# Optimization experiments

Measured on AMD Instinct MI355X. Metric: run time of the kernel, lower is better.

## Reference

```python
import jax, jax.numpy as jnp
import numpy as np

MAX_SHIFT = 64  # init kwarg; alpha=None -> score_max branch


def setup_inputs() -> dict:
    key = jax.random.key(0)
    k1, k2 = jax.random.split(key)
    x = jax.random.normal(k1, (64, 2, 4096), dtype=jnp.float32)
    y = jax.random.normal(k2, (64, 2, 4096), dtype=jnp.float32)
    return {"x": x, "y": y}


def reference(x, y):
    S = MAX_SHIFT
    W = 2 * S + 1  # num_windows
    # forward(): flip along channel axis
    x = jnp.flip(x, axis=1)
    B, C, D = x.shape
    # min-max normalize each (batch, channel) trace to [-1, 1]
    xmin = x.min(axis=-1, keepdims=True)
    xmax = x.max(axis=-1, keepdims=True)
    x = 2 * (x - xmin) / (xmax - xmin) - 1
    # torch.hann_window(dim) is periodic: 0.5*(1 - cos(2*pi*n/N))
    hann = 0.5 * (1.0 - jnp.cos(2.0 * jnp.pi * jnp.arange(D, dtype=x.dtype) / D))
    x = x * hann
    # pad by max_shift on both sides, then take W sliding windows of length D
    xpad = jnp.pad(x, ((0, 0), (0, 0), (S, S)))  # [B, C, D+2S]
    idx = jnp.arange(W)[:, None] + jnp.arange(D)[None, :]  # [W, D]
    xw = xpad[:, :, idx]  # [B, C, W, D] (matches torch unfold+reshape)
    xw = jnp.transpose(xw, (2, 0, 1, 3))  # [W, B, C, D]
    # mean-centered Pearson correlation per window
    xc = xw - xw.mean(axis=-1, keepdims=True)
    yc = y - y.mean(axis=-1, keepdims=True)
    corr = jnp.sum(xc * yc, axis=-1)  # [W, B, C]
    norm = jnp.sum(xc * xc, axis=-1) * jnp.sum(yc * yc, axis=-1)
    corr = corr / jnp.sqrt(norm)
    # alpha is None -> score_max: max over shifts, L2 over channels
    values = corr.max(axis=0)  # [B, C]
    scores = jnp.sqrt(jnp.sum(values ** 2, axis=-1))  # [B]
    return -scores.mean()
```

## Files before the change

### kernel.cpp

```cpp
#include <hip/hip_runtime.h>
#include <math.h>

#define DD      4096
#define WW      129
#define XSN     4240
#define BLOCKN  256
#define NBLK    512

__device__ float g_part[NBLK];
__device__ int   g_cnt = 0;

__global__ __launch_bounds__(BLOCKN) void spl_fused(
        const float* __restrict__ x, const float* __restrict__ y,
        float* __restrict__ out) {
    const int blk = blockIdx.x;
    const int bc  = blk >> 2, p = blk & 3;
    const int b   = bc >> 1,  c = bc & 1;
    const float* xp = x + (size_t)(b * 2 + (1 - c)) * DD;
    const float* yp = y + (size_t)(b * 2 + c) * DD;
    const float4* xp4 = (const float4*)xp;
    const float4* yp4 = (const float4*)yp;

    __shared__ __align__(16) float xs[XSN];
    __shared__ float P0s[65], P0q[65], Qs[65], Qq[65];
    __shared__ float red[16];
    __shared__ float wred[4];
    __shared__ int lastFlag;

    const int tid = threadIdx.x, lane = tid & 63, wv = tid >> 6;

    if (tid < 36) {
        int i4 = (tid < 16) ? tid : (1024 + tid);
        ((float4*)xs)[i4] = make_float4(0.f, 0.f, 0.f, 0.f);
    }

    float4 xv4[4];
    #pragma unroll
    for (int it = 0; it < 4; ++it) xv4[it] = xp4[tid + 256 * it];
    float4 yv4[16];
    #pragma unroll
    for (int i = 0; i < 16; ++i) yv4[i] = yp4[64 * i + lane];

    float4 h4[4];
    #pragma unroll
    for (int it = 0; it < 4; ++it) {
        float fd = (float)(4 * (tid + 256 * it));
        h4[it].x = 0.5f - 0.5f * __builtin_amdgcn_cosf((fd + 0.0f) * (1.0f / (float)DD));
        h4[it].y = 0.5f - 0.5f * __builtin_amdgcn_cosf((fd + 1.0f) * (1.0f / (float)DD));
        h4[it].z = 0.5f - 0.5f * __builtin_amdgcn_cosf((fd + 2.0f) * (1.0f / (float)DD));
        h4[it].w = 0.5f - 0.5f * __builtin_amdgcn_cosf((fd + 3.0f) * (1.0f / (float)DD));
    }

    float xmn = 3.0e38f, xmx = -3.0e38f;
    #pragma unroll
    for (int it = 0; it < 4; ++it) {
        float4 xv = xv4[it];
        xmn = fminf(xmn, fminf(fminf(xv.x, xv.y), fminf(xv.z, xv.w)));
        xmx = fmaxf(xmx, fmaxf(fmaxf(xv.x, xv.y), fmaxf(xv.z, xv.w)));
    }
    #pragma unroll
    for (int off = 32; off > 0; off >>= 1) {
        xmn = fminf(xmn, __shfl_down(xmn, off, 64));
        xmx = fmaxf(xmx, __shfl_down(xmx, off, 64));
    }
    if (lane == 0) { red[wv] = xmn; red[4 + wv] = xmx; }

    float ys0 = 0.0f, ys1 = 0.0f;
    #pragma unroll
    for (int i = 0; i < 16; i += 2) {
        ys0 += (yv4[i].x + yv4[i].y) + (yv4[i].z + yv4[i].w);
        ys1 += (yv4[i + 1].x + yv4[i + 1].y) + (yv4[i + 1].z + yv4[i + 1].w);
    }
    float ysum = ys0 + ys1;
    #pragma unroll
    for (int off = 32; off > 0; off >>= 1) ysum += __shfl_down(ysum, off, 64);
    ysum = __shfl(ysum, 0, 64);
    const float ymean = ysum * (1.0f / (float)DD);

    __syncthreads();
    xmn = fminf(fminf(red[0], red[1]), fminf(red[2], red[3]));
    xmx = fmaxf(fmaxf(red[4], red[5]), fmaxf(red[6], red[7]));
    const float a   = 2.0f / (xmx - xmn);
    const float bsh = -a * xmn - 1.0f;

    float ssum = 0.0f, ssq = 0.0f;
    #pragma unroll
    for (int it = 0; it < 4; ++it) {
        int i4 = tid + 256 * it;
        float4 v;
        v.x = fmaf(a, xv4[it].x, bsh) * h4[it].x;
        v.y = fmaf(a, xv4[it].y, bsh) * h4[it].y;
        v.z = fmaf(a, xv4[it].z, bsh) * h4[it].z;
        v.w = fmaf(a, xv4[it].w, bsh) * h4[it].w;
        ((float4*)(xs + 64))[i4] = v;
        ssum += (v.x + v.y) + (v.z + v.w);
        ssq = fmaf(v.x, v.x, fmaf(v.y, v.y, fmaf(v.z, v.z, fmaf(v.w, v.w, ssq))));
    }
    #pragma unroll
    for (int off = 32; off > 0; off >>= 1) {
        ssum += __shfl_down(ssum, off, 64);
        ssq  += __shfl_down(ssq,  off, 64);
    }
    if (lane == 0) { red[8 + wv] = ssum; red[12 + wv] = ssq; }

    float sy0 = 0.0f, sy1 = 0.0f;
    #pragma unroll
    for (int i = 0; i < 16; ++i) {
        yv4[i].x -= ymean; yv4[i].y -= ymean; yv4[i].z -= ymean; yv4[i].w -= ymean;
        float* acc = (i & 1) ? &sy1 : &sy0;
        *acc = fmaf(yv4[i].x, yv4[i].x, fmaf(yv4[i].y, yv4[i].y,
               fmaf(yv4[i].z, yv4[i].z, fmaf(yv4[i].w, yv4[i].w, *acc))));
    }
    float syy = sy0 + sy1;
    #pragma unroll
    for (int off = 32; off > 0; off >>= 1) syy += __shfl_down(syy, off, 64);
    syy = __shfl(syy, 0, 64);

    if (wv == 0) {
        int d = lane;
        float h = 0.5f - 0.5f * __builtin_amdgcn_cosf((float)d * (1.0f / (float)DD));
        float v = fmaf(a, xp[d], bsh) * h;
        float s = v, sq = v * v;
        #pragma unroll
        for (int off = 1; off < 64; off <<= 1) {
            float t  = __shfl_up(s,  off, 64);
            float tq = __shfl_up(sq, off, 64);
            if (lane >= off) { s += t; sq += tq; }
        }
        P0s[lane + 1] = s; P0q[lane + 1] = sq;
        if (lane == 0) { P0s[0] = 0.0f; P0q[0] = 0.0f; }
    } else if (wv == 1) {
        int d = 4032 + lane;
        float h = 0.5f - 0.5f * __builtin_amdgcn_cosf((float)d * (1.0f / (float)DD));
        float v = fmaf(a, xp[d], bsh) * h;
        float s = v, sq = v * v;
        #pragma unroll
        for (int off = 1; off < 64; off <<= 1) {
            float t  = __shfl_up(s,  off, 64);
            float tq = __shfl_up(sq, off, 64);
            if (lane >= off) { s += t; sq += tq; }
        }
        float Ts = __shfl(s, 63, 64), Tq = __shfl(sq, 63, 64);
        Qs[lane] = Ts - (s - v);
        Qq[lane] = Tq - (sq - v * v);
        if (lane == 63) { Qs[64] = 0.0f; Qq[64] = 0.0f; }
    }
    __syncthreads();
    const float Stot  = (red[8]  + red[9])  + (red[10] + red[11]);
    const float Sqtot = (red[12] + red[13]) + (red[14] + red[15]);

    const float4* xs4 = (const float4*)xs;
    float vmax = -3.0e38f;
    for (int g = p + 4 * wv; g <= 16; g += 16) {
        float cr[8];
        #pragma unroll
        for (int j = 0; j < 8; ++j) cr[j] = 0.0f;
        const int A0 = lane + 2 * g;
        #pragma unroll
        for (int i = 0; i < 16; ++i) {
            int A = 64 * i + A0;
            float4 x0 = xs4[A], x1 = xs4[A + 1], x2 = xs4[A + 2];
            float wnd[12] = { x0.x, x0.y, x0.z, x0.w,
                              x1.x, x1.y, x1.z, x1.w,
                              x2.x, x2.y, x2.z, x2.w };
            float4 yv = yv4[i];
            #pragma unroll
            for (int j = 0; j < 8; ++j)
                cr[j] = fmaf(yv.x, wnd[j],
                        fmaf(yv.y, wnd[j + 1],
                        fmaf(yv.z, wnd[j + 2],
                        fmaf(yv.w, wnd[j + 3], cr[j]))));
        }
        #pragma unroll
        for (int off = 32; off > 0; off >>= 1) {
            #pragma unroll
            for (int j = 0; j < 8; ++j) cr[j] += __shfl_down(cr[j], off, 64);
        }
        if (lane == 0) {
            #pragma unroll
            for (int j = 0; j < 8; ++j) {
                int w = 8 * g + j;
                if (w < WW) {
                    int hidx = (w > 64) ? (w - 64) : 0;
                    int tidx = (w < 64) ? w : 64;
                    float sx   = Stot  - P0s[hidx] - Qs[tidx];
                    float sxx  = Sqtot - P0q[hidx] - Qq[tidx];
                    float varx = sxx - sx * sx * (1.0f / (float)DD);
                    float corr = cr[j] / sqrtf(varx * syy);
                    vmax = fmaxf(vmax, corr);
                }
            }
        }
    }
    if (lane == 0) wred[wv] = vmax;
    __syncthreads();

    if (tid == 0) {
        float bm = fmaxf(fmaxf(wred[0], wred[1]), fmaxf(wred[2], wred[3]));
        __hip_atomic_store(&g_part[blk], bm, __ATOMIC_RELEASE,
                           __HIP_MEMORY_SCOPE_AGENT);
        int old = __hip_atomic_fetch_add(&g_cnt, 1, __ATOMIC_ACQ_REL,
                                         __HIP_MEMORY_SCOPE_AGENT);
        lastFlag = (old == NBLK - 1) ? 1 : 0;
    }
    __syncthreads();
    if (lastFlag != 0 && wv == 0) {
        const int bb = lane;
        float v0 = -3.0e38f, v1 = -3.0e38f;
        #pragma unroll
        for (int pp = 0; pp < 4; ++pp) {
            v0 = fmaxf(v0, __hip_atomic_load(&g_part[(bb * 2 + 0) * 4 + pp],
                            __ATOMIC_RELAXED, __HIP_MEMORY_SCOPE_AGENT));
            v1 = fmaxf(v1, __hip_atomic_load(&g_part[(bb * 2 + 1) * 4 + pp],
                            __ATOMIC_RELAXED, __HIP_MEMORY_SCOPE_AGENT));
        }
        float s = sqrtf(v0 * v0 + v1 * v1);
        #pragma unroll
        for (int off = 32; off > 0; off >>= 1) s += __shfl_down(s, off, 64);
        if (lane == 0) {
            out[0] = -s * (1.0f / 64.0f);
            __hip_atomic_store(&g_cnt, 0, __ATOMIC_RELAXED,
                               __HIP_MEMORY_SCOPE_AGENT);
        }
    }
}

extern "C" void kernel_launch(void* const* d_in, const int* in_sizes, int n_in,
                              void* d_out, int out_size, void* d_ws, size_t ws_size,
                              hipStream_t stream) {
    const float* x = (const float*)d_in[0];
    const float* y = (const float*)d_in[1];
    float* out     = (float*)d_out;
    (void)d_ws; (void)ws_size;

    spl_fused<<<dim3(NBLK), dim3(BLOCKN), 0, stream>>>(x, y, out);
}
```

Before: 77.72 us.

## Split fused kernel into main and final reduction kernels, recompute Hann inline

Drops the atomic counter and last-block reduction and writes per-block maxima to workspace, which a second one-block kernel then reduces. The Hann window is now computed inside the normalize loop instead of being precomputed into registers, lowering register pressure. This removes the device-scope atomics and release/acquire fences but adds a second kernel launch and a global round trip for the partials.

```diff
diff --git a/kernel.cpp b/kernel.cpp
--- a/kernel.cpp
+++ b/kernel.cpp
@@ -4,15 +4,12 @@
 #define DD      4096
 #define WW      129
 #define XSN     4240
+#define NP      4
 #define BLOCKN  256
-#define NBLK    512
-
-__device__ float g_part[NBLK];
-__device__ int   g_cnt = 0;
-
-__global__ __launch_bounds__(BLOCKN) void spl_fused(
+
+__global__ __launch_bounds__(BLOCKN) void spl_main(
         const float* __restrict__ x, const float* __restrict__ y,
-        float* __restrict__ out) {
+        float* __restrict__ partial) {
     const int blk = blockIdx.x;
     const int bc  = blk >> 2, p = blk & 3;
     const int b   = bc >> 1,  c = bc & 1;
@@ -25,7 +22,6 @@
     __shared__ float P0s[65], P0q[65], Qs[65], Qq[65];
     __shared__ float red[16];
     __shared__ float wred[4];
-    __shared__ int lastFlag;
 
     const int tid = threadIdx.x, lane = tid & 63, wv = tid >> 6;
 
@@ -40,16 +36,6 @@
     float4 yv4[16];
     #pragma unroll
     for (int i = 0; i < 16; ++i) yv4[i] = yp4[64 * i + lane];
-
-    float4 h4[4];
-    #pragma unroll
-    for (int it = 0; it < 4; ++it) {
-        float fd = (float)(4 * (tid + 256 * it));
-        h4[it].x = 0.5f - 0.5f * __builtin_amdgcn_cosf((fd + 0.0f) * (1.0f / (float)DD));
-        h4[it].y = 0.5f - 0.5f * __builtin_amdgcn_cosf((fd + 1.0f) * (1.0f / (float)DD));
-        h4[it].z = 0.5f - 0.5f * __builtin_amdgcn_cosf((fd + 2.0f) * (1.0f / (float)DD));
-        h4[it].w = 0.5f - 0.5f * __builtin_amdgcn_cosf((fd + 3.0f) * (1.0f / (float)DD));
-    }
 
     float xmn = 3.0e38f, xmx = -3.0e38f;
     #pragma unroll
@@ -87,11 +73,16 @@
     #pragma unroll
     for (int it = 0; it < 4; ++it) {
         int i4 = tid + 256 * it;
+        float fd = (float)(4 * i4);
         float4 v;
-        v.x = fmaf(a, xv4[it].x, bsh) * h4[it].x;
-        v.y = fmaf(a, xv4[it].y, bsh) * h4[it].y;
-        v.z = fmaf(a, xv4[it].z, bsh) * h4[it].z;
-        v.w = fmaf(a, xv4[it].w, bsh) * h4[it].w;
+        v.x = fmaf(a, xv4[it].x, bsh) *
+              (0.5f - 0.5f * __builtin_amdgcn_cosf((fd + 0.0f) * (1.0f / (float)DD)));
+        v.y = fmaf(a, xv4[it].y, bsh) *
+              (0.5f - 0.5f * __builtin_amdgcn_cosf((fd + 1.0f) * (1.0f / (float)DD)));
+        v.z = fmaf(a, xv4[it].z, bsh) *
+              (0.5f - 0.5f * __builtin_amdgcn_cosf((fd + 2.0f) * (1.0f / (float)DD)));
+        v.w = fmaf(a, xv4[it].w, bsh) *
+              (0.5f - 0.5f * __builtin_amdgcn_cosf((fd + 3.0f) * (1.0f / (float)DD)));
         ((float4*)(xs + 64))[i4] = v;
         ssum += (v.x + v.y) + (v.z + v.w);
         ssq = fmaf(v.x, v.x, fmaf(v.y, v.y, fmaf(v.z, v.z, fmaf(v.w, v.w, ssq))));
@@ -194,35 +185,23 @@
     }
     if (lane == 0) wred[wv] = vmax;
     __syncthreads();
-
-    if (tid == 0) {
-        float bm = fmaxf(fmaxf(wred[0], wred[1]), fmaxf(wred[2], wred[3]));
-        __hip_atomic_store(&g_part[blk], bm, __ATOMIC_RELEASE,
-                           __HIP_MEMORY_SCOPE_AGENT);
-        int old = __hip_atomic_fetch_add(&g_cnt, 1, __ATOMIC_ACQ_REL,
-                                         __HIP_MEMORY_SCOPE_AGENT);
-        lastFlag = (old == NBLK - 1) ? 1 : 0;
-    }
-    __syncthreads();
-    if (lastFlag != 0 && wv == 0) {
-        const int bb = lane;
-        float v0 = -3.0e38f, v1 = -3.0e38f;
-        #pragma unroll
-        for (int pp = 0; pp < 4; ++pp) {
-            v0 = fmaxf(v0, __hip_atomic_load(&g_part[(bb * 2 + 0) * 4 + pp],
-                            __ATOMIC_RELAXED, __HIP_MEMORY_SCOPE_AGENT));
-            v1 = fmaxf(v1, __hip_atomic_load(&g_part[(bb * 2 + 1) * 4 + pp],
-                            __ATOMIC_RELAXED, __HIP_MEMORY_SCOPE_AGENT));
-        }
-        float s = sqrtf(v0 * v0 + v1 * v1);
-        #pragma unroll
-        for (int off = 32; off > 0; off >>= 1) s += __shfl_down(s, off, 64);
-        if (lane == 0) {
-            out[0] = -s * (1.0f / 64.0f);
-            __hip_atomic_store(&g_cnt, 0, __ATOMIC_RELAXED,
-                               __HIP_MEMORY_SCOPE_AGENT);
-        }
-    }
+    if (tid == 0)
+        partial[blk] = fmaxf(fmaxf(wred[0], wred[1]), fmaxf(wred[2], wred[3]));
+}
+
+__global__ void spl_final(const float* __restrict__ partial,
+                          float* __restrict__ out) {
+    const int b = threadIdx.x;
+    float v0 = -3.0e38f, v1 = -3.0e38f;
+    #pragma unroll
+    for (int pp = 0; pp < NP; ++pp) {
+        v0 = fmaxf(v0, partial[(b * 2 + 0) * NP + pp]);
+        v1 = fmaxf(v1, partial[(b * 2 + 1) * NP + pp]);
+    }
+    float s = sqrtf(v0 * v0 + v1 * v1);
+    #pragma unroll
+    for (int off = 32; off > 0; off >>= 1) s += __shfl_down(s, off, 64);
+    if (b == 0) out[0] = -s * (1.0f / 64.0f);
 }
 
 extern "C" void kernel_launch(void* const* d_in, const int* in_sizes, int n_in,
@@ -231,7 +210,8 @@
     const float* x = (const float*)d_in[0];
     const float* y = (const float*)d_in[1];
     float* out     = (float*)d_out;
-    (void)d_ws; (void)ws_size;
-
-    spl_fused<<<dim3(NBLK), dim3(BLOCKN), 0, stream>>>(x, y, out);
+    float* partial = (float*)d_ws;
+
+    spl_main<<<dim3(128 * NP), dim3(BLOCKN), 0, stream>>>(x, y, partial);
+    spl_final<<<dim3(1), dim3(64), 0, stream>>>(partial, out);
 }
```

After: 68.48 us. -11.9%, faster.
